# Optimization experiments

Hardware: AMD Instinct MI355X
Metric: run time of the kernel (lower is better)

The kernel has to match this reference:

```python
import jax, jax.numpy as jnp
import numpy as np
import math

# dims matching init_kwargs
B, N, CS, CZ = 1, 512, 384, 128
H, C, PQ, PV = 8, 128, 8, 8
INF, EPS = 1e5, 1e-8

# ---- quaternion / motor helpers (PGA motor encoded as [qw,qx,qy,qz,tx,ty,tz,0]) ----

def quat_conj(q):
    return q * jnp.array([1.0, -1.0, -1.0, -1.0], q.dtype)

def quat_mul(a, b):
    aw, ax, ay, az = jnp.split(a, 4, -1)
    bw, bx, by, bz = jnp.split(b, 4, -1)
    return jnp.concatenate([
        aw*bw - ax*bx - ay*by - az*bz,
        aw*bx + ax*bw + ay*bz - az*by,
        aw*by - ax*bz + ay*bw + az*bx,
        aw*bz + ax*by - ay*bx + az*bw], -1)

def quat_rotate(q, v):
    qv = q[..., 1:]
    uv = jnp.cross(qv, v)
    uuv = jnp.cross(qv, uv)
    return v + 2.0 * (q[..., :1] * uv + uuv)

def point_trafo(p, q, t):
    # p [...,K,3]; rigid transform by frame motor, homogeneous 4-vector out
    pp = quat_rotate(q, p) + t
    return jnp.concatenate([pp, jnp.ones_like(pp[..., :1])], -1)

def mv_transform(mv, q, t):
    # versor sandwich on a 16-dim multivector: three rotatable 3-vector blocks,
    # the point block (7:10, weight at 10) also translates; slots 0 and 10:16 invariant
    s0 = mv[..., 0:1]
    v1 = quat_rotate(q, mv[..., 1:4])
    v2 = quat_rotate(q, mv[..., 4:7])
    w = mv[..., 10:11]
    p = quat_rotate(q, mv[..., 7:10]) + w * t
    return jnp.concatenate([s0, v1, v2, p, mv[..., 10:16]], -1)

def mv_transform_inv(mv, q, t):
    qc = quat_conj(q)
    s0 = mv[..., 0:1]
    v1 = quat_rotate(qc, mv[..., 1:4])
    v2 = quat_rotate(qc, mv[..., 4:7])
    w = mv[..., 10:11]
    p = quat_rotate(qc, mv[..., 7:10] - w * t)
    return jnp.concatenate([s0, v1, v2, p, mv[..., 10:16]], -1)


def _forward(s, g, z, T, mask, W_q, b_q, W_kv, b_kv, W_qp, b_qp, W_kp, b_kp,
             W_vg, b_vg, W_mg, W_b, b_b, W_dz, b_dz, head_weights,
             softmax_weights, W_out, b_out, W_geo):
    T8 = T[..., :8]                                      # extract_motor
    qn = T8[..., :4]
    qn = qn / jnp.sqrt(jnp.sum(qn**2, -1, keepdims=True) + EPS)
    tr = T8[..., 4:7]

    q = (s @ W_q + b_q).reshape(B, N, H, C)
    kv = (s @ W_kv + b_kv).reshape(B, N, H, 2 * C)
    k, v = kv[..., :C], kv[..., C:]

    def make_pts(W, bb):
        # split into 3 chunks + stack(dim=-1) == reshape(...,3,HP).swapaxes
        p = (s @ W + bb).reshape(B, N, 3, H * PQ).swapaxes(-1, -2)  # [B,N,HP,3]
        p4 = point_trafo(p, qn[:, :, None, :], tr[:, :, None, :])
        return p4.reshape(B, N, H, PQ, 4)

    q_pts = make_pts(W_qp, b_qp)
    k_pts = make_pts(W_kp, b_kp)

    v_g = (s @ W_vg + b_vg).reshape(B, N, PV, 16)
    v_g = jnp.einsum('oi,bnic->bnoc', W_mg,
                     jnp.concatenate([v_g, g], -2)).reshape(B, N, H, PV, 16)

    bias = jnp.einsum('bijz,zh->bhij', z, W_b) + b_b[None, :, None, None]
    a = jnp.einsum('bihc,bjhc->bhij', q, k) * math.sqrt(1.0 / (3 * C))
    a = a + math.sqrt(1.0 / 3.0) * bias

    disp = q_pts[:, :, None, :, :, :3] - k_pts[:, None, :, :, :, :3]  # [B,N,N,H,P,3]
    pt = jnp.sum(disp**2, -1)                                         # [B,N,N,H,P]
    hw = jax.nn.softplus(head_weights) * math.sqrt(1.0 / (3 * (PQ * 9.0 / 2)))
    pt = -0.5 * jnp.sum(pt * hw[None, None, None, :, None], -1)       # [B,N,N,H]

    sq_mask = INF * (mask[:, :, None] * mask[:, None, :] - 1.0)
    a = a + pt.transpose(0, 3, 1, 2) + sq_mask[:, None]
    a = jax.nn.softmax(softmax_weights[None, :, None, None] * a, axis=-1)

    o = jnp.einsum('bhij,bjhc->bihc', a, v)                           # [B,N,H,C]

    qb, tb = qn[:, :, None, None, :], tr[:, :, None, None, :]
    vg_glob = mv_transform(v_g, qb, tb)
    o_g = jnp.einsum('bhij,bjhpc->bihpc', a, vg_glob)
    o_g = mv_transform_inv(o_g, qb, tb)                               # [B,N,H,PV,16]
    n1 = jnp.sqrt(jnp.sum(o_g[..., :10]**2, -1) + EPS)
    n2 = jnp.sqrt(jnp.sum(o_g[..., 10:]**2, -1) + EPS)
    o_g_norm = jnp.stack([n1, n2], -1)                                # [B,N,H,PV,2]

    # local relative frame features (8 per head)
    q_rel = quat_mul(quat_conj(qn)[:, :, None, :], qn[:, None, :, :])
    t_rel = quat_rotate(quat_conj(qn)[:, :, None, :], tr[:, None, :, :] - tr[:, :, None, :])
    rel = jnp.concatenate([q_rel, t_rel, jnp.zeros_like(t_rel[..., :1])], -1)  # [B,N,N,8]
    o_rel = jnp.einsum('bhij,bijc->bihc', a, rel)

    o_pair = jnp.einsum('bhij,bijc->bihc', a, z @ W_dz + b_dz)        # [B,N,H,CZ//4]

    feats = jnp.concatenate([o_pair, o, o_rel,
                             o_g.reshape(B, N, H, PV * 16),
                             o_g_norm.reshape(B, N, H, PV * 2)], -1).reshape(B, N, -1)
    s_out = feats @ W_out + b_out                                     # [B,N,CS]
    g_out = jnp.einsum('oi,bnic->bnoc', W_geo, o_g.reshape(B, N, H * PV, 16))
    return s_out, g_out


def setup_inputs() -> dict:
    key = jax.random.key(0)
    ks = jax.random.split(key, 32)
    def rn(i, shape, sc=1.0):
        return sc * jax.random.normal(ks[i], shape, jnp.float32)
    s = rn(0, (B, N, CS))
    g = rn(1, (B, N, PV, 16))
    z = rn(2, (B, N, N, CZ))
    Traw = rn(3, (B, N, 16))
    qn = Traw[..., :4]
    qn = qn / jnp.sqrt(jnp.sum(qn**2, -1, keepdims=True) + 1e-8)
    T = Traw.at[..., :4].set(qn).at[..., 4:7].multiply(3.0).at[..., 7:].set(0.0)
    mask = jnp.ones((B, N), jnp.float32)
    w = 0.02
    CAT = H * (CZ // 4 + C + 8 + PV * 18)   # 2496
    return dict(
        s=s, g=g, z=z, T=T, mask=mask,
        W_q=rn(4, (CS, H * C), w), b_q=jnp.zeros((H * C,), jnp.float32),
        W_kv=rn(5, (CS, 2 * H * C), w), b_kv=jnp.zeros((2 * H * C,), jnp.float32),
        W_qp=rn(6, (CS, H * PQ * 3), w), b_qp=jnp.zeros((H * PQ * 3,), jnp.float32),
        W_kp=rn(7, (CS, H * PQ * 3), w), b_kp=jnp.zeros((H * PQ * 3,), jnp.float32),
        W_vg=rn(8, (CS, PV * 16), w), b_vg=jnp.zeros((PV * 16,), jnp.float32),
        W_mg=rn(9, (H * PV, 2 * PV), 0.1),
        W_b=rn(10, (CZ, H), w), b_b=jnp.zeros((H,), jnp.float32),
        W_dz=rn(11, (CZ, CZ // 4), w), b_dz=jnp.zeros((CZ // 4,), jnp.float32),
        head_weights=-2.0 + 0.3 * rn(12, (H,)),
        softmax_weights=jnp.ones((H,), jnp.float32) + 0.1 * rn(13, (H,)),
        W_out=rn(14, (CAT, CS), w), b_out=jnp.zeros((CS,), jnp.float32),
        W_geo=rn(15, (PV, H * PV), 0.1))


def reference(s, g, z, T, mask, W_q, b_q, W_kv, b_kv, W_qp, b_qp, W_kp, b_kp,
              W_vg, b_vg, W_mg, W_b, b_b, W_dz, b_dz, head_weights,
              softmax_weights, W_out, b_out, W_geo):
    return _forward(s, g, z, T, mask, W_q, b_q, W_kv, b_kv, W_qp, b_qp, W_kp,
                    b_kp, W_vg, b_vg, W_mg, W_b, b_b, W_dz, b_dz, head_weights,
                    softmax_weights, W_out, b_out, W_geo)
```

## Files before the change

### kernel.cpp

```cpp
#include <hip/hip_runtime.h>
#include <math.h>

#define NN 512
#define CSD 384
#define CZD 128
#define HD 8
#define CD 128
#define EPSV 1e-8f
#define INFV 100000.0f

#define OFF_QN    ((size_t)0)
#define OFF_TR    ((size_t)2048)
#define OFF_ROWT  ((size_t)4096)
#define OFF_COLT  ((size_t)8192)
#define OFF_SB    ((size_t)12288)
#define OFF_QBUF  ((size_t)45056)
#define OFF_KV    ((size_t)569344)
#define OFF_QPR   ((size_t)1617920)
#define OFF_KPR   ((size_t)1716224)
#define OFF_VGR   ((size_t)1814528)
#define OFF_ZB    ((size_t)1880064)
#define OFF_A     ((size_t)3977216)
#define OFF_AMH   ((size_t)6074368)
#define OFF_AML   ((size_t)7122944)
#define OFF_UH    ((size_t)8171520)
#define OFF_UL    ((size_t)8499200)
#define OFF_VH    ((size_t)8826880)
#define OFF_VL    ((size_t)9154560)
#define OFF_VPH   ((size_t)9482240)
#define OFF_VPL   ((size_t)10006528)
#define OFF_OB0   ((size_t)10530816)
#define OFF_OB1   ((size_t)11055104)
#define OFF_OG0   ((size_t)11579392)
#define OFF_OG1   ((size_t)12103680)
#define OFF_FH    ((size_t)12627968)
#define OFF_FL    ((size_t)13266944)
#define OFF_PS    ((size_t)13905920)
#define OFF_SH    ((size_t)15085568)
#define OFF_SL    ((size_t)15183872)
#define OFF_WTH   ((size_t)15282176)
#define OFF_WTL   ((size_t)15970304)
#define OFF_WOH   ((size_t)16658432)
#define OFF_WOL   ((size_t)17137664)
#define OFF_AZP   ((size_t)17616896)

typedef __attribute__((ext_vector_type(4))) float f32x4;
typedef __attribute__((ext_vector_type(8))) short bf16x8;
typedef __attribute__((ext_vector_type(4))) short s16x4;
typedef unsigned short u16;

__device__ __forceinline__ void qrot(const float q[4], const float* v, float* out) {
    float qw = q[0], qx = q[1], qy = q[2], qz = q[3];
    float ux = qy*v[2] - qz*v[1];
    float uy = qz*v[0] - qx*v[2];
    float uz = qx*v[1] - qy*v[0];
    float uux = qy*uz - qz*uy;
    float uuy = qz*ux - qx*uz;
    float uuz = qx*uy - qy*ux;
    out[0] = v[0] + 2.0f*(qw*ux + uux);
    out[1] = v[1] + 2.0f*(qw*uy + uuy);
    out[2] = v[2] + 2.0f*(qw*uz + uuz);
}

__device__ __forceinline__ void cvt2(float x, u16& h, u16& lo) {
    unsigned u = __float_as_uint(x);
    unsigned r = (u + 0x7FFFu + ((u >> 16) & 1u)) >> 16;
    h = (u16)r;
    float hf = __uint_as_float(r << 16);
    float lf = x - hf;
    unsigned u2 = __float_as_uint(lf);
    unsigned r2 = (u2 + 0x7FFFu + ((u2 >> 16) & 1u)) >> 16;
    lo = (u16)r2;
}
__device__ __forceinline__ float bf2f(u16 h) { return __uint_as_float((unsigned)h << 16); }

#define MFMA3(acc, avh, avl, bvh, bvl) \
    acc = __builtin_amdgcn_mfma_f32_16x16x32_bf16(avh, bvh, acc, 0, 0, 0); \
    acc = __builtin_amdgcn_mfma_f32_16x16x32_bf16(avh, bvl, acc, 0, 0, 0); \
    acc = __builtin_amdgcn_mfma_f32_16x16x32_bf16(avl, bvh, acc, 0, 0, 0);


__global__ __launch_bounds__(256) void k_split(
    const float* __restrict__ s, const float* __restrict__ W_q, const float* __restrict__ W_kv,
    const float* __restrict__ W_qp, const float* __restrict__ W_kp, const float* __restrict__ W_vg,
    const float* __restrict__ W_out,
    u16* __restrict__ sh_, u16* __restrict__ sl_,
    u16* __restrict__ WTh, u16* __restrict__ WTl,
    u16* __restrict__ WOh, u16* __restrict__ WOl)
{
    __shared__ float tile[64*68];
    int task = blockIdx.z, bx = blockIdx.x, by = blockIdx.y, t = threadIdx.x;
    if (task == 0) {
        if (by >= 6) return;
        const float* W; int ldn, sn0;
        if (bx < 16)      { W = W_q;  ldn = 1024; sn0 = bx*64; }
        else if (bx < 48) { W = W_kv; ldn = 2048; sn0 = (bx-16)*64; }
        else if (bx < 51) { W = W_qp; ldn = 192;  sn0 = (bx-48)*64; }
        else if (bx < 54) { W = W_kp; ldn = 192;  sn0 = (bx-51)*64; }
        else              { W = W_vg; ldn = 128;  sn0 = (bx-54)*64; }
        int k0 = by*64;
        #pragma unroll
        for (int lp = 0; lp < 4; lp++) {
            int kk = (t>>4) + lp*16, nn = (t&15)*4;
            float4 v = *(const float4*)(W + (size_t)(k0+kk)*ldn + sn0 + nn);
            tile[kk*68+nn]=v.x; tile[kk*68+nn+1]=v.y; tile[kk*68+nn+2]=v.z; tile[kk*68+nn+3]=v.w;
        }
        __syncthreads();
        #pragma unroll
        for (int lp = 0; lp < 4; lp++) {
            int nn = (t>>4) + lp*16, kk4 = (t&15)*4;
            s16x4 vh, vl;
            #pragma unroll
            for (int e = 0; e < 4; e++) {
                u16 h, lo; cvt2(tile[(kk4+e)*68 + nn], h, lo);
                vh[e] = (short)h; vl[e] = (short)lo;
            }
            size_t o = (size_t)(bx*64 + nn)*384 + k0 + kk4;
            *(s16x4*)(WTh + o) = vh;
            *(s16x4*)(WTl + o) = vl;
        }
    } else if (task == 1) {
        if (bx >= 6 || by >= 39) return;
        int n0 = bx*64, k0 = by*64;
        #pragma unroll
        for (int lp = 0; lp < 4; lp++) {
            int kk = (t>>4) + lp*16, nn = (t&15)*4;
            float4 v = *(const float4*)(W_out + (size_t)(k0+kk)*384 + n0 + nn);
            tile[kk*68+nn]=v.x; tile[kk*68+nn+1]=v.y; tile[kk*68+nn+2]=v.z; tile[kk*68+nn+3]=v.w;
        }
        __syncthreads();
        #pragma unroll
        for (int lp = 0; lp < 4; lp++) {
            int nn = (t>>4) + lp*16, kk4 = (t&15)*4;
            s16x4 vh, vl;
            #pragma unroll
            for (int e = 0; e < 4; e++) {
                u16 h, lo; cvt2(tile[(kk4+e)*68 + nn], h, lo);
                vh[e] = (short)h; vl[e] = (short)lo;
            }
            size_t o = (size_t)(n0 + nn)*2496 + k0 + kk4;
            *(s16x4*)(WOh + o) = vh;
            *(s16x4*)(WOl + o) = vl;
        }
    } else {
        if (bx >= 8 || by >= 6) return;
        int m0 = bx*64, k0 = by*64;
        #pragma unroll
        for (int lp = 0; lp < 4; lp++) {
            int row = (t>>4) + lp*16, c4 = (t&15)*4;
            float4 v = *(const float4*)(s + (size_t)(m0+row)*384 + k0 + c4);
            s16x4 vh, vl;
            u16 h, lo;
            cvt2(v.x,h,lo); vh[0]=(short)h; vl[0]=(short)lo;
            cvt2(v.y,h,lo); vh[1]=(short)h; vl[1]=(short)lo;
            cvt2(v.z,h,lo); vh[2]=(short)h; vl[2]=(short)lo;
            cvt2(v.w,h,lo); vh[3]=(short)h; vl[3]=(short)lo;
            size_t o = (size_t)(m0+row)*384 + k0 + c4;
            *(s16x4*)(sh_ + o) = vh;
            *(s16x4*)(sl_ + o) = vl;
        }
    }
}

__global__ __launch_bounds__(256) void k_proj_all(
    const u16* __restrict__ sh_, const u16* __restrict__ sl_,
    const u16* __restrict__ WTh, const u16* __restrict__ WTl,
    const float* __restrict__ b_q,  float* __restrict__ qbuf,
    const float* __restrict__ b_kv, float* __restrict__ kvb,
    const float* __restrict__ b_qp, float* __restrict__ qpr,
    const float* __restrict__ b_kp, float* __restrict__ kpr,
    const float* __restrict__ b_vg, float* __restrict__ vgr)
{
    int ny = blockIdx.y;
    const float* bias; float* C; int N, n0, base;
    if (ny < 16)      { bias=b_q;  C=qbuf; N=1024; n0=ny*64;      base=0; }
    else if (ny < 48) { bias=b_kv; C=kvb;  N=2048; n0=(ny-16)*64; base=1024; }
    else if (ny < 51) { bias=b_qp; C=qpr;  N=192;  n0=(ny-48)*64; base=3072; }
    else if (ny < 54) { bias=b_kp; C=kpr;  N=192;  n0=(ny-51)*64; base=3264; }
    else              { bias=b_vg; C=vgr;  N=128;  n0=(ny-54)*64; base=3456; }
    int m0 = blockIdx.x*64;
    int t = threadIdx.x, w = t>>6, l = t&63, g = l>>4, li = l&15;
    const u16* Ah = sh_ + (size_t)(m0 + w*16 + li)*384 + g*8;
    const u16* Al = sl_ + (size_t)(m0 + w*16 + li)*384 + g*8;
    const u16* Bh0 = WTh + (size_t)(base + n0 + li)*384 + g*8;
    const u16* Bl0 = WTl + (size_t)(base + n0 + li)*384 + g*8;
    f32x4 acc[4] = {};
    for (int ks = 0; ks < 12; ks++) {
        bf16x8 avh = *(const bf16x8*)(Ah + ks*32);
        bf16x8 avl = *(const bf16x8*)(Al + ks*32);
        #pragma unroll
        for (int c = 0; c < 4; c++) {
            bf16x8 bvh = *(const bf16x8*)(Bh0 + (size_t)c*16*384 + ks*32);
            bf16x8 bvl = *(const bf16x8*)(Bl0 + (size_t)c*16*384 + ks*32);
            MFMA3(acc[c], avh, avl, bvh, bvl);
        }
    }
    #pragma unroll
    for (int c = 0; c < 4; c++) {
        int col = n0 + c*16 + li;
        float bb = bias[col];
        #pragma unroll
        for (int r = 0; r < 4; r++) {
            int row = m0 + w*16 + g*4 + r;
            C[(size_t)row*N + col] = acc[c][r] + bb;
        }
    }
}

__global__ __launch_bounds__(256) void k_geo(
    const float* __restrict__ T,
    const float* __restrict__ qpr, const float* __restrict__ kpr,
    const float* __restrict__ vgr, const float* __restrict__ g,
    const float* __restrict__ W_mg,
    const float* __restrict__ qbuf, const float* __restrict__ kvb,
    const float* __restrict__ hwraw, const float* __restrict__ b_b,
    float* __restrict__ qn, float* __restrict__ tr,
    u16* __restrict__ Uh, u16* __restrict__ Ul,
    u16* __restrict__ Vh, u16* __restrict__ Vl,
    float* __restrict__ rowt, float* __restrict__ colt,
    u16* __restrict__ Vph, u16* __restrict__ Vpl)
{
    __shared__ float s_q[4];
    __shared__ float s_t[3];
    __shared__ float s_qpts[192], s_kpts[192];
    __shared__ float s_Qsq[8], s_Ksq[8];
    int n = blockIdx.x, t = threadIdx.x;
    if (t == 0) {
        float q0=T[n*16+0], q1=T[n*16+1], q2=T[n*16+2], q3=T[n*16+3];
        float inv = 1.0f/sqrtf(q0*q0+q1*q1+q2*q2+q3*q3 + EPSV);
        float a0=q0*inv, a1=q1*inv, a2=q2*inv, a3=q3*inv;
        s_q[0]=a0; s_q[1]=a1; s_q[2]=a2; s_q[3]=a3;
        float u0=T[n*16+4], u1=T[n*16+5], u2=T[n*16+6];
        s_t[0]=u0; s_t[1]=u1; s_t[2]=u2;
        qn[n*4+0]=a0; qn[n*4+1]=a1; qn[n*4+2]=a2; qn[n*4+3]=a3;
        tr[n*3+0]=u0; tr[n*3+1]=u1; tr[n*3+2]=u2;
    }
    __syncthreads();
    float q[4]={s_q[0],s_q[1],s_q[2],s_q[3]};
    float t0=s_t[0], t1=s_t[1], t2=s_t[2];
    if (t < 128) {
        int m = t & 63;
        const float* raw = (t < 64) ? qpr : kpr;
        float p[3] = {raw[n*192 + m], raw[n*192 + 64 + m], raw[n*192 + 128 + m]};
        float r[3]; qrot(q,p,r);
        r[0]+=t0; r[1]+=t1; r[2]+=t2;
        float* dp = (t<64) ? s_qpts : s_kpts;
        dp[m*3+0]=r[0]; dp[m*3+1]=r[1]; dp[m*3+2]=r[2];
        float ss = r[0]*r[0]+r[1]*r[1]+r[2]*r[2];
        ss += __shfl_down(ss,4,8);
        ss += __shfl_down(ss,2,8);
        ss += __shfl_down(ss,1,8);
        if ((m&7)==0) ((t<64)?s_Qsq:s_Ksq)[m>>3] = ss;
    } else if (t < 192) {
        int o = t - 128;
        float in[16];
        #pragma unroll
        for (int c=0;c<16;c++){
            float acc=0.0f;
            #pragma unroll
            for (int i=0;i<8;i++)  acc += W_mg[o*16+i]*vgr[n*128+i*16+c];
            #pragma unroll
            for (int i=8;i<16;i++) acc += W_mg[o*16+i]*g[n*128+(i-8)*16+c];
            in[c]=acc;
        }
        float out[16];
        out[0]=in[0];
        qrot(q,in+1,out+1);
        qrot(q,in+4,out+4);
        float w=in[10];
        qrot(q,in+7,out+7);
        out[7]+=w*t0; out[8]+=w*t1; out[9]+=w*t2;
        #pragma unroll
        for (int c=10;c<16;c++) out[c]=in[c];
        int h=o>>3, pp=o&7;
        size_t vb = ((size_t)(h*512+n))*256 + 128 + pp*16;
        #pragma unroll
        for (int c=0;c<16;c++) {
            u16 hh, ll; cvt2(out[c], hh, ll);
            Vph[vb+c]=hh; Vpl[vb+c]=ll;
        }
    }
    #pragma unroll
    for (int l=0;l<4;l++){
        int f = t + l*256; int h = f>>7, c = f&127;
        u16 hh, ll; cvt2(kvb[(size_t)n*2048 + h*256 + 128 + c], hh, ll);
        Vph[((size_t)(h*512+n))*256 + c] = hh;
        Vpl[((size_t)(h*512+n))*256 + c] = ll;
    }
    __syncthreads();
    #pragma unroll
    for (int h = 0; h < 8; h++) {
        float hwv = log1pf(expf(hwraw[h])) * 0.09622504486493763f;
        if (t < 160) {
            float u, v;
            if (t < 128) {
                u = 0.05103103630798287f * qbuf[(size_t)n*1024 + h*128 + t];
                v = kvb[(size_t)n*2048 + h*256 + t];
            } else if (t < 152) {
                int d = t - 128;
                u = hwv * s_qpts[h*24 + d];
                v = s_kpts[h*24 + d];
            } else { u = 0.0f; v = 0.0f; }
            size_t o = ((size_t)h*512 + n)*160 + t;
            u16 hh, ll;
            cvt2(u, hh, ll); Uh[o]=hh; Ul[o]=ll;
            cvt2(v, hh, ll); Vh[o]=hh; Vl[o]=ll;
        }
        if (t == 160) rowt[h*512+n] = -0.5f*hwv*s_Qsq[h] + 0.5773502691896258f*b_b[h] - INFV;
        if (t == 161) colt[h*512+n] = -0.5f*hwv*s_Ksq[h];
    }
}

__global__ __launch_bounds__(256) void k_zb(const float* __restrict__ z,
        const float* __restrict__ W_b, float* __restrict__ zb) {
    int i = blockIdx.x, j0 = blockIdx.y*128;
    int t = threadIdx.x, w = t>>6, l = t&63;
    int jj = l>>5, c4 = (l&31)<<2;
    float wb[4][8];
    #pragma unroll
    for (int e=0;e<4;e++)
        #pragma unroll
        for (int h=0;h<8;h++) wb[e][h] = W_b[(c4+e)*8 + h];
    int jbase = j0 + w*32 + jj;
    const float* zp = z + ((size_t)i*512 + jbase)*128 + c4;
    for (int k = 0; k < 16; k++) {
        float4 v = *(const float4*)(zp + (size_t)k*256);
        float acc[8];
        #pragma unroll
        for (int h=0;h<8;h++)
            acc[h] = v.x*wb[0][h] + v.y*wb[1][h] + v.z*wb[2][h] + v.w*wb[3][h];
        #pragma unroll
        for (int h=0;h<8;h++) {
            #pragma unroll
            for (int m=16;m>0;m>>=1) acc[h] += __shfl_xor(acc[h], m);
        }
        if ((l&31) < 8) {
            int h = l&31;
            zb[((size_t)h*512 + i)*512 + jbase + k*2] = acc[h];
        }
    }
}

__global__ __launch_bounds__(256) void k_scorefill(
        const u16* __restrict__ Uh, const u16* __restrict__ Ul,
        const u16* __restrict__ Vh, const u16* __restrict__ Vl,
        const float* __restrict__ rowt, const float* __restrict__ colt,
        const float* __restrict__ zb, const float* __restrict__ mask,
        const float* __restrict__ sw, float* __restrict__ Am) {
    int h = blockIdx.z;
    int m0 = blockIdx.x*64, n0 = blockIdx.y*64;
    int t = threadIdx.x, w = t>>6, l = t&63, g = l>>4, li = l&15;
    const u16* Ah = Uh + ((size_t)h*512 + m0 + w*16 + li)*160 + g*8;
    const u16* Al = Ul + ((size_t)h*512 + m0 + w*16 + li)*160 + g*8;
    const u16* Bh0 = Vh + ((size_t)h*512 + n0 + li)*160 + g*8;
    const u16* Bl0 = Vl + ((size_t)h*512 + n0 + li)*160 + g*8;
    f32x4 acc[4] = {};
    #pragma unroll
    for (int ks = 0; ks < 5; ks++) {
        bf16x8 avh = *(const bf16x8*)(Ah + ks*32);
        bf16x8 avl = *(const bf16x8*)(Al + ks*32);
        #pragma unroll
        for (int c = 0; c < 4; c++) {
            bf16x8 bvh = *(const bf16x8*)(Bh0 + (size_t)c*16*160 + ks*32);
            bf16x8 bvl = *(const bf16x8*)(Bl0 + (size_t)c*16*160 + ks*32);
            MFMA3(acc[c], avh, avl, bvh, bvl);
        }
    }
    float swh = sw[h];
    #pragma unroll
    for (int c = 0; c < 4; c++) {
        int j = n0 + c*16 + li;
        float ct = colt[h*512 + j];
        float mj = mask[j];
        #pragma unroll
        for (int r = 0; r < 4; r++) {
            int i = m0 + w*16 + g*4 + r;
            float rt = rowt[h*512 + i];
            float mi = mask[i]*INFV;
            float zv = zb[((size_t)h*512 + i)*512 + j];
            Am[((size_t)h*512 + i)*512 + j] =
                (acc[c][r] + rt + ct + 0.5773502691896258f*zv + mi*mj)*swh;
        }
    }
}

__global__ __launch_bounds__(256) void k_softmax(const float* __restrict__ Am,
        u16* __restrict__ Amh, u16* __restrict__ Aml,
        const float* __restrict__ qn, const float* __restrict__ tr, float* __restrict__ S) {
    __shared__ float red[8];
    __shared__ float sred[4][8];
    int row = blockIdx.x;
    const float* p = Am + (size_t)row*512;
    int t = threadIdx.x;
    float x0 = p[t], x1 = p[t+256];
    float m = fmaxf(x0, x1);
    #pragma unroll
    for (int o = 32; o > 0; o >>= 1) m = fmaxf(m, __shfl_xor(m, o));
    int wv = t >> 6, ln = t & 63;
    if (ln == 0) red[wv] = m;
    __syncthreads();
    m = fmaxf(fmaxf(red[0], red[1]), fmaxf(red[2], red[3]));
    float e0 = expf(x0 - m), e1 = expf(x1 - m);
    float sm = e0 + e1;
    #pragma unroll
    for (int o = 32; o > 0; o >>= 1) sm += __shfl_xor(sm, o);
    __syncthreads();
    if (ln == 0) red[4 + wv] = sm;
    __syncthreads();
    float inv = 1.0f / (red[4]+red[5]+red[6]+red[7]);
    float a0 = e0*inv, a1 = e1*inv;
    u16 hh, ll;
    cvt2(a0, hh, ll); Amh[(size_t)row*512 + t] = hh;     Aml[(size_t)row*512 + t] = ll;
    cvt2(a1, hh, ll); Amh[(size_t)row*512 + t+256] = hh; Aml[(size_t)row*512 + t+256] = ll;
    float4 q0 = *(const float4*)(qn + t*4);
    float4 q1 = *(const float4*)(qn + (t+256)*4);
    float acc[8];
    acc[0] = a0*q0.x + a1*q1.x;
    acc[1] = a0*q0.y + a1*q1.y;
    acc[2] = a0*q0.z + a1*q1.z;
    acc[3] = a0*q0.w + a1*q1.w;
    acc[4] = a0*tr[t*3+0] + a1*tr[(t+256)*3+0];
    acc[5] = a0*tr[t*3+1] + a1*tr[(t+256)*3+1];
    acc[6] = a0*tr[t*3+2] + a1*tr[(t+256)*3+2];
    acc[7] = a0 + a1;
    #pragma unroll
    for (int c = 0; c < 8; c++) {
        #pragma unroll
        for (int o = 32; o > 0; o >>= 1) acc[c] += __shfl_xor(acc[c], o);
    }
    if (ln == 0) {
        #pragma unroll
        for (int c = 0; c < 8; c++) sred[wv][c] = acc[c];
    }
    __syncthreads();
    if (t < 8) {
        int h = row >> 9, i = row & 511;
        S[i*64 + h*8 + t] = sred[0][t]+sred[1][t]+sred[2][t]+sred[3][t];
    }
}

__global__ __launch_bounds__(256) void k_az(
        const u16* __restrict__ Amh, const u16* __restrict__ Aml,
        const float* __restrict__ z, float* __restrict__ azp) {
    __shared__ float aT[128*12];
    __shared__ float part[3*1024];
    int i = blockIdx.x, jq = blockIdx.y, j0 = jq*128;
    int t = threadIdx.x;
    #pragma unroll
    for (int l2 = 0; l2 < 4; l2++) {
        int f = t + l2*256;
        int h = f >> 7, jl = f & 127;
        size_t idx = ((size_t)h*512 + i)*512 + j0 + jl;
        aT[jl*12 + h] = bf2f(Amh[idx]) + bf2f(Aml[idx]);
    }
    __syncthreads();
    int c2 = t & 63, sub = t >> 6;
    int jb = sub*32;
    float acc[8][2] = {};
    for (int jo = 0; jo < 32; jo++) {
        int j = jb + jo;
        float2 zv = *(const float2*)(z + ((size_t)i*512 + j0 + j)*128 + c2*2);
        float4 a0 = *(const float4*)(aT + j*12);
        float4 a1 = *(const float4*)(aT + j*12 + 4);
        acc[0][0] += a0.x*zv.x; acc[0][1] += a0.x*zv.y;
        acc[1][0] += a0.y*zv.x; acc[1][1] += a0.y*zv.y;
        acc[2][0] += a0.z*zv.x; acc[2][1] += a0.z*zv.y;
        acc[3][0] += a0.w*zv.x; acc[3][1] += a0.w*zv.y;
        acc[4][0] += a1.x*zv.x; acc[4][1] += a1.x*zv.y;
        acc[5][0] += a1.y*zv.x; acc[5][1] += a1.y*zv.y;
        acc[6][0] += a1.z*zv.x; acc[6][1] += a1.z*zv.y;
        acc[7][0] += a1.w*zv.x; acc[7][1] += a1.w*zv.y;
    }
    if (sub > 0) {
        #pragma unroll
        for (int h = 0; h < 8; h++) {
            part[(sub-1)*1024 + h*128 + c2*2 + 0] = acc[h][0];
            part[(sub-1)*1024 + h*128 + c2*2 + 1] = acc[h][1];
        }
    }
    __syncthreads();
    if (sub == 0) {
        float* dst = azp + ((size_t)jq*512 + i)*1024;
        #pragma unroll
        for (int h = 0; h < 8; h++) {
            #pragma unroll
            for (int d = 0; d < 2; d++) {
                dst[h*128 + c2*2 + d] = acc[h][d] + part[h*128 + c2*2 + d]
                          + part[1024 + h*128 + c2*2 + d] + part[2048 + h*128 + c2*2 + d];
            }
        }
    }
}

__global__ __launch_bounds__(256) void k_apply(
        const u16* __restrict__ Amh, const u16* __restrict__ Aml,
        const u16* __restrict__ Vph, const u16* __restrict__ Vpl,
        float* __restrict__ ob0, float* __restrict__ ob1,
        float* __restrict__ og0, float* __restrict__ og1) {
    __shared__ u16 sBh[2][64*48];
    __shared__ u16 sBl[2][64*48];
    int m0 = blockIdx.x*64;
    int n0 = blockIdx.y*64;
    int h = blockIdx.z & 7, js = blockIdx.z >> 3;
    int t = threadIdx.x, w = t>>6, l = t&63, g = l>>4, li = l&15;
    int jl = t>>3, c8 = (t&7)*8;
    int jsw = jl ^ (((c8>>3)&3)<<3);
    const u16* Ah = Amh + ((size_t)h*512 + m0 + w*16 + li)*512 + js*256 + g*8;
    const u16* Al = Aml + ((size_t)h*512 + m0 + w*16 + li)*512 + js*256 + g*8;
    f32x4 acc[4] = {};
    {
        const u16* srcH = Vph + ((size_t)h*512 + js*256 + jl)*256 + n0 + c8;
        const u16* srcL = Vpl + ((size_t)h*512 + js*256 + jl)*256 + n0 + c8;
        bf16x8 vh = *(const bf16x8*)srcH;
        bf16x8 vl = *(const bf16x8*)srcL;
        #pragma unroll
        for (int e = 0; e < 8; e++) {
            sBh[0][(c8+e)*48 + jsw] = (u16)vh[e];
            sBl[0][(c8+e)*48 + jsw] = (u16)vl[e];
        }
    }
    __syncthreads();
    for (int kc = 0; kc < 8; kc++) {
        int cur = kc & 1;
        if (kc + 1 < 8) {
            int koff = js*256 + (kc+1)*32;
            const u16* srcH = Vph + ((size_t)h*512 + koff + jl)*256 + n0 + c8;
            const u16* srcL = Vpl + ((size_t)h*512 + koff + jl)*256 + n0 + c8;
            bf16x8 vh = *(const bf16x8*)srcH;
            bf16x8 vl = *(const bf16x8*)srcL;
            #pragma unroll
            for (int e = 0; e < 8; e++) {
                sBh[cur^1][(c8+e)*48 + jsw] = (u16)vh[e];
                sBl[cur^1][(c8+e)*48 + jsw] = (u16)vl[e];
            }
        }
        bf16x8 avh = *(const bf16x8*)(Ah + kc*32);
        bf16x8 avl = *(const bf16x8*)(Al + kc*32);
        #pragma unroll
        for (int c = 0; c < 4; c++) {
            int col = c*16 + li;
            int gp = g ^ ((col>>3)&3);
            bf16x8 bvh = *(const bf16x8*)(&sBh[cur][col*48 + gp*8]);
            bf16x8 bvl = *(const bf16x8*)(&sBl[cur][col*48 + gp*8]);
            MFMA3(acc[c], avh, avl, bvh, bvl);
        }
        __syncthreads();
    }
    float* obuf = js ? ob1 : ob0;
    float* og   = js ? og1 : og0;
    #pragma unroll
    for (int c = 0; c < 4; c++) {
        int col = n0 + c*16 + li;
        float* base = (col < 128) ? (obuf + h*128 + col) : (og + h*128 + col - 128);
        #pragma unroll
        for (int r = 0; r < 4; r++) {
            int i = m0 + w*16 + g*4 + r;
            base[(size_t)i*1024] = acc[c][r];
        }
    }
}

__global__ __launch_bounds__(256) void k_azfin(
    const float* __restrict__ azp,
    const float* __restrict__ ob0, const float* __restrict__ ob1,
    const float* __restrict__ og0, const float* __restrict__ og1,
    const float* __restrict__ W_dz, const float* __restrict__ b_dz,
    const float* __restrict__ S, const float* __restrict__ qn, const float* __restrict__ tr,
    const float* __restrict__ W_geo,
    u16* __restrict__ fh, u16* __restrict__ fl, float* __restrict__ outg)
{
    __shared__ float s_az[1024];
    __shared__ float s_og[1024];
    int i = blockIdx.x, t = threadIdx.x;
    #pragma unroll
    for (int l2 = 0; l2 < 4; l2++) {
        int c = t + l2*256;
        s_az[c] = azp[((size_t)0*512 + i)*1024 + c] + azp[((size_t)1*512 + i)*1024 + c]
                + azp[((size_t)2*512 + i)*1024 + c] + azp[((size_t)3*512 + i)*1024 + c];
    }
    __syncthreads();
    size_t fb = (size_t)i*2496;
    u16 hh, ll;
    #pragma unroll
    for (int l = 0; l < 4; l++) {
        int ff = t + l*256; int h = ff>>7, c = ff&127;
        float v = ob0[(size_t)i*1024 + h*128 + c] + ob1[(size_t)i*1024 + h*128 + c];
        cvt2(v, hh, ll); fh[fb + h*312 + 32 + c] = hh; fl[fb + h*312 + 32 + c] = ll;
    }
    {
        int h = t >> 5, cdz = t & 31;
        float a2 = b_dz[cdz];
        #pragma unroll 4
        for (int zc = 0; zc < 128; zc++) a2 += s_az[h*128 + zc]*W_dz[zc*32 + cdz];
        cvt2(a2, hh, ll); fh[fb + h*312 + cdz] = hh; fl[fb + h*312 + cdz] = ll;
    }
    float qc0=qn[i*4], qc1=-qn[i*4+1], qc2=-qn[i*4+2], qc3=-qn[i*4+3];
    float t0=tr[i*3], t1=tr[i*3+1], t2=tr[i*3+2];
    if (t < 64) {
        int h = t >> 3, p = t & 7;
        const float* a0 = og0 + (size_t)i*1024 + h*128 + p*16;
        const float* a1 = og1 + (size_t)i*1024 + h*128 + p*16;
        float in[16];
        #pragma unroll
        for (int c=0;c<16;c++) in[c]=a0[c]+a1[c];
        float qc[4]={qc0,qc1,qc2,qc3};
        float out[16];
        out[0]=in[0];
        qrot(qc,in+1,out+1);
        qrot(qc,in+4,out+4);
        float w=in[10];
        float tmp[3]={in[7]-w*t0, in[8]-w*t1, in[9]-w*t2};
        qrot(qc,tmp,out+7);
        #pragma unroll
        for (int c2x=10;c2x<16;c2x++) out[c2x]=in[c2x];
        float n1=EPSV, n2=EPSV;
        #pragma unroll
        for (int c2x=0;c2x<10;c2x++) n1 += out[c2x]*out[c2x];
        #pragma unroll
        for (int c2x=10;c2x<16;c2x++) n2 += out[c2x]*out[c2x];
        n1=sqrtf(n1); n2=sqrtf(n2);
        #pragma unroll
        for (int c2x=0;c2x<16;c2x++){
            cvt2(out[c2x], hh, ll);
            fh[fb + h*312+168+p*16+c2x] = hh; fl[fb + h*312+168+p*16+c2x] = ll;
            s_og[t*16+c2x]=out[c2x];
        }
        cvt2(n1, hh, ll); fh[fb + h*312+296+p*2]   = hh; fl[fb + h*312+296+p*2]   = ll;
        cvt2(n2, hh, ll); fh[fb + h*312+296+p*2+1] = hh; fl[fb + h*312+296+p*2+1] = ll;
    } else if (t < 72) {
        int h = t - 64;
        const float* Sr = S + i*64 + h*8;
        float b0=Sr[0], b1=Sr[1], b2=Sr[2], b3=Sr[3];
        float o0 = qc0*b0 - qc1*b1 - qc2*b2 - qc3*b3;
        float o1 = qc0*b1 + qc1*b0 + qc2*b3 - qc3*b2;
        float o2 = qc0*b2 - qc1*b3 + qc2*b0 + qc3*b1;
        float o3 = qc0*b3 + qc1*b2 - qc2*b1 + qc3*b0;
        float A = Sr[7];
        float v[3]={Sr[4]-A*t0, Sr[5]-A*t1, Sr[6]-A*t2};
        float qc[4]={qc0,qc1,qc2,qc3};
        float r[3]; qrot(qc,v,r);
        cvt2(o0,hh,ll);  fh[fb+h*312+160]=hh; fl[fb+h*312+160]=ll;
        cvt2(o1,hh,ll);  fh[fb+h*312+161]=hh; fl[fb+h*312+161]=ll;
        cvt2(o2,hh,ll);  fh[fb+h*312+162]=hh; fl[fb+h*312+162]=ll;
        cvt2(o3,hh,ll);  fh[fb+h*312+163]=hh; fl[fb+h*312+163]=ll;
        cvt2(r[0],hh,ll);fh[fb+h*312+164]=hh; fl[fb+h*312+164]=ll;
        cvt2(r[1],hh,ll);fh[fb+h*312+165]=hh; fl[fb+h*312+165]=ll;
        cvt2(r[2],hh,ll);fh[fb+h*312+166]=hh; fl[fb+h*312+166]=ll;
        fh[fb+h*312+167]=0; fl[fb+h*312+167]=0;
    }
    __syncthreads();
    if (t < 128) {
        int o = (t>>4) & 7, c = t & 15;
        float a3 = 0.0f;
        #pragma unroll 4
        for (int i2=0;i2<64;i2++) a3 += W_geo[o*64+i2]*s_og[i2*16+c];
        outg[(size_t)i*128 + o*16 + c] = a3;
    }
}

__global__ __launch_bounds__(256) void k_sout(
        const u16* __restrict__ fh, const u16* __restrict__ fl,
        const u16* __restrict__ WOh, const u16* __restrict__ WOl,
        float* __restrict__ Ps) {
    int m0 = blockIdx.x*64, n0 = blockIdx.y*64, kz = blockIdx.z;
    int t = threadIdx.x, w = t>>6, l = t&63, g = l>>4, li = l&15;
    const u16* Ah = fh + (size_t)(m0 + w*16 + li)*2496 + kz*416 + g*8;
    const u16* Al = fl + (size_t)(m0 + w*16 + li)*2496 + kz*416 + g*8;
    const u16* Bh0 = WOh + (size_t)(n0 + li)*2496 + kz*416 + g*8;
    const u16* Bl0 = WOl + (size_t)(n0 + li)*2496 + kz*416 + g*8;
    f32x4 acc[4] = {};
    for (int ks = 0; ks < 13; ks++) {
        bf16x8 avh = *(const bf16x8*)(Ah + ks*32);
        bf16x8 avl = *(const bf16x8*)(Al + ks*32);
        #pragma unroll
        for (int c = 0; c < 4; c++) {
            bf16x8 bvh = *(const bf16x8*)(Bh0 + (size_t)c*16*2496 + ks*32);
            bf16x8 bvl = *(const bf16x8*)(Bl0 + (size_t)c*16*2496 + ks*32);
            MFMA3(acc[c], avh, avl, bvh, bvl);
        }
    }
    float* slab = Ps + (size_t)kz*512*384;
    #pragma unroll
    for (int c = 0; c < 4; c++) {
        int col = n0 + c*16 + li;
        #pragma unroll
        for (int r = 0; r < 4; r++) {
            int row = m0 + w*16 + g*4 + r;
            slab[(size_t)row*CSD + col] = acc[c][r];
        }
    }
}

__global__ __launch_bounds__(256) void k_sout_red(const float* __restrict__ Ps,
        const float* __restrict__ b_out, float* __restrict__ out) {
    int idx = (blockIdx.x*256 + threadIdx.x)*4;
    float4 s = *(const float4*)(b_out + (idx % 384));
    #pragma unroll
    for (int kz = 0; kz < 6; kz++) {
        float4 p = *(const float4*)(Ps + (size_t)kz*196608 + idx);
        s.x += p.x; s.y += p.y; s.z += p.z; s.w += p.w;
    }
    *(float4*)(out + idx) = s;
}


extern "C" void kernel_launch(void* const* d_in, const int* in_sizes, int n_in,
                              void* d_out, int out_size, void* d_ws, size_t ws_size,
                              hipStream_t stream) {
    const float* s     = (const float*)d_in[0];
    const float* g     = (const float*)d_in[1];
    const float* z     = (const float*)d_in[2];
    const float* T     = (const float*)d_in[3];
    const float* mask  = (const float*)d_in[4];
    const float* W_q   = (const float*)d_in[5];
    const float* b_q   = (const float*)d_in[6];
    const float* W_kv  = (const float*)d_in[7];
    const float* b_kv  = (const float*)d_in[8];
    const float* W_qp  = (const float*)d_in[9];
    const float* b_qp  = (const float*)d_in[10];
    const float* W_kp  = (const float*)d_in[11];
    const float* b_kp  = (const float*)d_in[12];
    const float* W_vg  = (const float*)d_in[13];
    const float* b_vg  = (const float*)d_in[14];
    const float* W_mg  = (const float*)d_in[15];
    const float* W_b   = (const float*)d_in[16];
    const float* b_b   = (const float*)d_in[17];
    const float* W_dz  = (const float*)d_in[18];
    const float* b_dz  = (const float*)d_in[19];
    const float* hw    = (const float*)d_in[20];
    const float* sw    = (const float*)d_in[21];
    const float* W_out = (const float*)d_in[22];
    const float* b_out = (const float*)d_in[23];
    const float* W_geo = (const float*)d_in[24];

    float* ws   = (float*)d_ws;
    float* out  = (float*)d_out;

    float* qn   = ws + OFF_QN;
    float* tr   = ws + OFF_TR;
    float* rowt = ws + OFF_ROWT;
    float* colt = ws + OFF_COLT;
    float* Sbuf = ws + OFF_SB;
    float* qbuf = ws + OFF_QBUF;
    float* kvb  = ws + OFF_KV;
    float* qpr  = ws + OFF_QPR;
    float* kpr  = ws + OFF_KPR;
    float* vgr  = ws + OFF_VGR;
    float* zb   = ws + OFF_ZB;
    float* Am   = ws + OFF_A;
    u16* Amh    = (u16*)(ws + OFF_AMH);
    u16* Aml    = (u16*)(ws + OFF_AML);
    u16* Uh     = (u16*)(ws + OFF_UH);
    u16* Ul     = (u16*)(ws + OFF_UL);
    u16* Vh     = (u16*)(ws + OFF_VH);
    u16* Vl     = (u16*)(ws + OFF_VL);
    u16* Vph    = (u16*)(ws + OFF_VPH);
    u16* Vpl    = (u16*)(ws + OFF_VPL);
    float* ob0  = ws + OFF_OB0;
    float* ob1  = ws + OFF_OB1;
    float* og0  = ws + OFF_OG0;
    float* og1  = ws + OFF_OG1;
    u16* fh     = (u16*)(ws + OFF_FH);
    u16* fl     = (u16*)(ws + OFF_FL);
    float* Ps   = ws + OFF_PS;
    u16* sh_    = (u16*)(ws + OFF_SH);
    u16* sl_    = (u16*)(ws + OFF_SL);
    u16* WTh    = (u16*)(ws + OFF_WTH);
    u16* WTl    = (u16*)(ws + OFF_WTL);
    u16* WOh    = (u16*)(ws + OFF_WOH);
    u16* WOl    = (u16*)(ws + OFF_WOL);
    float* azp  = ws + OFF_AZP;

    k_split<<<dim3(56,39,3),256,0,stream>>>(s,W_q,W_kv,W_qp,W_kp,W_vg,W_out,
                                            sh_,sl_,WTh,WTl,WOh,WOl);
    k_proj_all<<<dim3(8,56),256,0,stream>>>(sh_,sl_,WTh,WTl,
                                            b_q,qbuf, b_kv,kvb, b_qp,qpr, b_kp,kpr, b_vg,vgr);
    k_geo<<<NN,256,0,stream>>>(T,qpr,kpr,vgr,g,W_mg,qbuf,kvb,hw,b_b,
                               qn,tr,Uh,Ul,Vh,Vl,rowt,colt,Vph,Vpl);
    k_zb<<<dim3(512,4),256,0,stream>>>(z,W_b,zb);
    k_scorefill<<<dim3(8,8,8),256,0,stream>>>(Uh,Ul,Vh,Vl,rowt,colt,zb,mask,sw,Am);
    k_softmax<<<4096,256,0,stream>>>(Am,Amh,Aml,qn,tr,Sbuf);
    k_az<<<dim3(512,4),256,0,stream>>>(Amh,Aml,z,azp);
    k_apply<<<dim3(8,4,16),256,0,stream>>>(Amh,Aml,Vph,Vpl,ob0,ob1,og0,og1);
    k_azfin<<<NN,256,0,stream>>>(azp,ob0,ob1,og0,og1,W_dz,b_dz,Sbuf,qn,tr,W_geo,
                                 fh,fl, out + (size_t)NN*CSD);
    k_sout<<<dim3(8,6,6),256,0,stream>>>(fh,fl,WOh,WOl,Ps);
    k_sout_red<<<192,256,0,stream>>>(Ps,b_out,out);
}
```

Before: 415.5 us.

## Fuse all stages into one cooperative persistent kernel with grid syncs

```diff
diff --git a/kernel.cpp b/kernel.cpp
--- a/kernel.cpp
+++ b/kernel.cpp
@@ -1,5 +1,8 @@
 #include <hip/hip_runtime.h>
+#include <hip/hip_cooperative_groups.h>
 #include <math.h>
+
+namespace cg = cooperative_groups;
 
 #define NN 512
 #define CSD 384
@@ -49,6 +52,14 @@
 typedef __attribute__((ext_vector_type(4))) short s16x4;
 typedef unsigned short u16;
 
+struct MegaP {
+    const float *s, *g, *z, *T, *mask;
+    const float *W_q, *b_q, *W_kv, *b_kv, *W_qp, *b_qp, *W_kp, *b_kp, *W_vg, *b_vg;
+    const float *W_mg, *W_b, *b_b, *W_dz, *b_dz, *hw, *sw, *W_out, *b_out, *W_geo;
+    float *ws;
+    float *out;
+};
+
 __device__ __forceinline__ void qrot(const float q[4], const float* v, float* out) {
     float qw = q[0], qx = q[1], qy = q[2], qz = q[3];
     float ux = qy*v[2] - qz*v[1];
@@ -80,24 +91,21 @@
     acc = __builtin_amdgcn_mfma_f32_16x16x32_bf16(avl, bvh, acc, 0, 0, 0);
 
 
-__global__ __launch_bounds__(256) void k_split(
-    const float* __restrict__ s, const float* __restrict__ W_q, const float* __restrict__ W_kv,
-    const float* __restrict__ W_qp, const float* __restrict__ W_kp, const float* __restrict__ W_vg,
-    const float* __restrict__ W_out,
-    u16* __restrict__ sh_, u16* __restrict__ sl_,
-    u16* __restrict__ WTh, u16* __restrict__ WTl,
-    u16* __restrict__ WOh, u16* __restrict__ WOl)
-{
-    __shared__ float tile[64*68];
-    int task = blockIdx.z, bx = blockIdx.x, by = blockIdx.y, t = threadIdx.x;
+__device__ void d_split(const MegaP& p, int task, int bx, int by, float* tile) {
+    int t = threadIdx.x;
+    u16* sh_ = (u16*)(p.ws + OFF_SH);
+    u16* sl_ = (u16*)(p.ws + OFF_SL);
+    u16* WTh = (u16*)(p.ws + OFF_WTH);
+    u16* WTl = (u16*)(p.ws + OFF_WTL);
+    u16* WOh = (u16*)(p.ws + OFF_WOH);
+    u16* WOl = (u16*)(p.ws + OFF_WOL);
     if (task == 0) {
-        if (by >= 6) return;
         const float* W; int ldn, sn0;
-        if (bx < 16)      { W = W_q;  ldn = 1024; sn0 = bx*64; }
-        else if (bx < 48) { W = W_kv; ldn = 2048; sn0 = (bx-16)*64; }
-        else if (bx < 51) { W = W_qp; ldn = 192;  sn0 = (bx-48)*64; }
-        else if (bx < 54) { W = W_kp; ldn = 192;  sn0 = (bx-51)*64; }
-        else              { W = W_vg; ldn = 128;  sn0 = (bx-54)*64; }
+        if (bx < 16)      { W = p.W_q;  ldn = 1024; sn0 = bx*64; }
+        else if (bx < 48) { W = p.W_kv; ldn = 2048; sn0 = (bx-16)*64; }
+        else if (bx < 51) { W = p.W_qp; ldn = 192;  sn0 = (bx-48)*64; }
+        else if (bx < 54) { W = p.W_kp; ldn = 192;  sn0 = (bx-51)*64; }
+        else              { W = p.W_vg; ldn = 128;  sn0 = (bx-54)*64; }
         int k0 = by*64;
         #pragma unroll
         for (int lp = 0; lp < 4; lp++) {
@@ -115,17 +123,16 @@
                 u16 h, lo; cvt2(tile[(kk4+e)*68 + nn], h, lo);
                 vh[e] = (short)h; vl[e] = (short)lo;
             }
-            size_t o = (size_t)(bx*64 + nn)*384 + k0 + kk4;
+            size_t o = (size_t)(bx*64 + nn)*384 + by*64 + kk4;
             *(s16x4*)(WTh + o) = vh;
             *(s16x4*)(WTl + o) = vl;
         }
     } else if (task == 1) {
-        if (bx >= 6 || by >= 39) return;
         int n0 = bx*64, k0 = by*64;
         #pragma unroll
         for (int lp = 0; lp < 4; lp++) {
             int kk = (t>>4) + lp*16, nn = (t&15)*4;
-            float4 v = *(const float4*)(W_out + (size_t)(k0+kk)*384 + n0 + nn);
+            float4 v = *(const float4*)(p.W_out + (size_t)(k0+kk)*384 + n0 + nn);
             tile[kk*68+nn]=v.x; tile[kk*68+nn+1]=v.y; tile[kk*68+nn+2]=v.z; tile[kk*68+nn+3]=v.w;
         }
         __syncthreads();
@@ -143,12 +150,11 @@
             *(s16x4*)(WOl + o) = vl;
         }
     } else {
-        if (bx >= 8 || by >= 6) return;
         int m0 = bx*64, k0 = by*64;
         #pragma unroll
         for (int lp = 0; lp < 4; lp++) {
             int row = (t>>4) + lp*16, c4 = (t&15)*4;
-            float4 v = *(const float4*)(s + (size_t)(m0+row)*384 + k0 + c4);
+            float4 v = *(const float4*)(p.s + (size_t)(m0+row)*384 + k0 + c4);
             s16x4 vh, vl;
             u16 h, lo;
             cvt2(v.x,h,lo); vh[0]=(short)h; vl[0]=(short)lo;
@@ -162,23 +168,48 @@
     }
 }
 
-__global__ __launch_bounds__(256) void k_proj_all(
-    const u16* __restrict__ sh_, const u16* __restrict__ sl_,
-    const u16* __restrict__ WTh, const u16* __restrict__ WTl,
-    const float* __restrict__ b_q,  float* __restrict__ qbuf,
-    const float* __restrict__ b_kv, float* __restrict__ kvb,
-    const float* __restrict__ b_qp, float* __restrict__ qpr,
-    const float* __restrict__ b_kp, float* __restrict__ kpr,
-    const float* __restrict__ b_vg, float* __restrict__ vgr)
-{
-    int ny = blockIdx.y;
+__device__ void d_zb(const MegaP& p, int i, int jq) {
+    float* zb = p.ws + OFF_ZB;
+    int j0 = jq*128;
+    int t = threadIdx.x, w = t>>6, l = t&63;
+    int jj = l>>5, c4 = (l&31)<<2;
+    float wb[4][8];
+    #pragma unroll
+    for (int e=0;e<4;e++)
+        #pragma unroll
+        for (int h=0;h<8;h++) wb[e][h] = p.W_b[(c4+e)*8 + h];
+    int jbase = j0 + w*32 + jj;
+    const float* zp = p.z + ((size_t)i*512 + jbase)*128 + c4;
+    for (int k = 0; k < 16; k++) {
+        float4 v = *(const float4*)(zp + (size_t)k*256);
+        float acc[8];
+        #pragma unroll
+        for (int h=0;h<8;h++)
+            acc[h] = v.x*wb[0][h] + v.y*wb[1][h] + v.z*wb[2][h] + v.w*wb[3][h];
+        #pragma unroll
+        for (int h=0;h<8;h++) {
+            #pragma unroll
+            for (int m=16;m>0;m>>=1) acc[h] += __shfl_xor(acc[h], m);
+        }
+        if ((l&31) < 8) {
+            int h = l&31;
+            zb[((size_t)h*512 + i)*512 + jbase + k*2] = acc[h];
+        }
+    }
+}
+
+__device__ void d_proj(const MegaP& p, int bx, int ny) {
+    const u16* sh_ = (const u16*)(p.ws + OFF_SH);
+    const u16* sl_ = (const u16*)(p.ws + OFF_SL);
+    const u16* WTh = (const u16*)(p.ws + OFF_WTH);
+    const u16* WTl = (const u16*)(p.ws + OFF_WTL);
     const float* bias; float* C; int N, n0, base;
-    if (ny < 16)      { bias=b_q;  C=qbuf; N=1024; n0=ny*64;      base=0; }
-    else if (ny < 48) { bias=b_kv; C=kvb;  N=2048; n0=(ny-16)*64; base=1024; }
-    else if (ny < 51) { bias=b_qp; C=qpr;  N=192;  n0=(ny-48)*64; base=3072; }
-    else if (ny < 54) { bias=b_kp; C=kpr;  N=192;  n0=(ny-51)*64; base=3264; }
-    else              { bias=b_vg; C=vgr;  N=128;  n0=(ny-54)*64; base=3456; }
-    int m0 = blockIdx.x*64;
+    if (ny < 16)      { bias=p.b_q;  C=p.ws+OFF_QBUF; N=1024; n0=ny*64;      base=0; }
+    else if (ny < 48) { bias=p.b_kv; C=p.ws+OFF_KV;   N=2048; n0=(ny-16)*64; base=1024; }
+    else if (ny < 51) { bias=p.b_qp; C=p.ws+OFF_QPR;  N=192;  n0=(ny-48)*64; base=3072; }
+    else if (ny < 54) { bias=p.b_kp; C=p.ws+OFF_KPR;  N=192;  n0=(ny-51)*64; base=3264; }
+    else              { bias=p.b_vg; C=p.ws+OFF_VGR;  N=128;  n0=(ny-54)*64; base=3456; }
+    int m0 = bx*64;
     int t = threadIdx.x, w = t>>6, l = t&63, g = l>>4, li = l&15;
     const u16* Ah = sh_ + (size_t)(m0 + w*16 + li)*384 + g*8;
     const u16* Al = sl_ + (size_t)(m0 + w*16 + li)*384 + g*8;
@@ -207,30 +238,28 @@
     }
 }
 
-__global__ __launch_bounds__(256) void k_geo(
-    const float* __restrict__ T,
-    const float* __restrict__ qpr, const float* __restrict__ kpr,
-    const float* __restrict__ vgr, const float* __restrict__ g,
-    const float* __restrict__ W_mg,
-    const float* __restrict__ qbuf, const float* __restrict__ kvb,
-    const float* __restrict__ hwraw, const float* __restrict__ b_b,
-    float* __restrict__ qn, float* __restrict__ tr,
-    u16* __restrict__ Uh, u16* __restrict__ Ul,
-    u16* __restrict__ Vh, u16* __restrict__ Vl,
-    float* __restrict__ rowt, float* __restrict__ colt,
-    u16* __restrict__ Vph, u16* __restrict__ Vpl)
-{
-    __shared__ float s_q[4];
-    __shared__ float s_t[3];
-    __shared__ float s_qpts[192], s_kpts[192];
-    __shared__ float s_Qsq[8], s_Ksq[8];
-    int n = blockIdx.x, t = threadIdx.x;
+__device__ void d_geo(const MegaP& p, int n, float* sg) {
+    float* s_q = sg; float* s_t = sg+4;
+    float* s_qpts = sg+8; float* s_kpts = sg+200;
+    float* s_Qsq = sg+392; float* s_Ksq = sg+400;
+    const float* qpr = p.ws + OFF_QPR;
+    const float* kpr = p.ws + OFF_KPR;
+    const float* vgr = p.ws + OFF_VGR;
+    const float* qbuf = p.ws + OFF_QBUF;
+    const float* kvb = p.ws + OFF_KV;
+    float* qn = p.ws + OFF_QN;
+    float* tr = p.ws + OFF_TR;
+    u16* Uh = (u16*)(p.ws + OFF_UH); u16* Ul = (u16*)(p.ws + OFF_UL);
+    u16* Vh = (u16*)(p.ws + OFF_VH); u16* Vl = (u16*)(p.ws + OFF_VL);
+    float* rowt = p.ws + OFF_ROWT; float* colt = p.ws + OFF_COLT;
+    u16* Vph = (u16*)(p.ws + OFF_VPH); u16* Vpl = (u16*)(p.ws + OFF_VPL);
+    int t = threadIdx.x;
     if (t == 0) {
-        float q0=T[n*16+0], q1=T[n*16+1], q2=T[n*16+2], q3=T[n*16+3];
+        float q0=p.T[n*16+0], q1=p.T[n*16+1], q2=p.T[n*16+2], q3=p.T[n*16+3];
         float inv = 1.0f/sqrtf(q0*q0+q1*q1+q2*q2+q3*q3 + EPSV);
         float a0=q0*inv, a1=q1*inv, a2=q2*inv, a3=q3*inv;
         s_q[0]=a0; s_q[1]=a1; s_q[2]=a2; s_q[3]=a3;
-        float u0=T[n*16+4], u1=T[n*16+5], u2=T[n*16+6];
+        float u0=p.T[n*16+4], u1=p.T[n*16+5], u2=p.T[n*16+6];
         s_t[0]=u0; s_t[1]=u1; s_t[2]=u2;
         qn[n*4+0]=a0; qn[n*4+1]=a1; qn[n*4+2]=a2; qn[n*4+3]=a3;
         tr[n*3+0]=u0; tr[n*3+1]=u1; tr[n*3+2]=u2;
@@ -241,8 +270,8 @@
     if (t < 128) {
         int m = t & 63;
         const float* raw = (t < 64) ? qpr : kpr;
-        float p[3] = {raw[n*192 + m], raw[n*192 + 64 + m], raw[n*192 + 128 + m]};
-        float r[3]; qrot(q,p,r);
+        float pp[3] = {raw[n*192 + m], raw[n*192 + 64 + m], raw[n*192 + 128 + m]};
+        float r[3]; qrot(q,pp,r);
         r[0]+=t0; r[1]+=t1; r[2]+=t2;
         float* dp = (t<64) ? s_qpts : s_kpts;
         dp[m*3+0]=r[0]; dp[m*3+1]=r[1]; dp[m*3+2]=r[2];
@@ -258,9 +287,9 @@
         for (int c=0;c<16;c++){
             float acc=0.0f;
             #pragma unroll
-            for (int i=0;i<8;i++)  acc += W_mg[o*16+i]*vgr[n*128+i*16+c];
+            for (int i2=0;i2<8;i2++)  acc += p.W_mg[o*16+i2]*vgr[n*128+i2*16+c];
             #pragma unroll
-            for (int i=8;i<16;i++) acc += W_mg[o*16+i]*g[n*128+(i-8)*16+c];
+            for (int i2=8;i2<16;i2++) acc += p.W_mg[o*16+i2]*p.g[n*128+(i2-8)*16+c];
             in[c]=acc;
         }
         float out[16];
@@ -272,8 +301,8 @@
         out[7]+=w*t0; out[8]+=w*t1; out[9]+=w*t2;
         #pragma unroll
         for (int c=10;c<16;c++) out[c]=in[c];
-        int h=o>>3, pp=o&7;
-        size_t vb = ((size_t)(h*512+n))*256 + 128 + pp*16;
+        int h=o>>3, pp2=o&7;
+        size_t vb = ((size_t)(h*512+n))*256 + 128 + pp2*16;
         #pragma unroll
         for (int c=0;c<16;c++) {
             u16 hh, ll; cvt2(out[c], hh, ll);
@@ -290,7 +319,7 @@
     __syncthreads();
     #pragma unroll
     for (int h = 0; h < 8; h++) {
-        float hwv = log1pf(expf(hwraw[h])) * 0.09622504486493763f;
+        float hwv = log1pf(expf(p.hw[h])) * 0.09622504486493763f;
         if (t < 160) {
             float u, v;
             if (t < 128) {
@@ -306,49 +335,21 @@
             cvt2(u, hh, ll); Uh[o]=hh; Ul[o]=ll;
             cvt2(v, hh, ll); Vh[o]=hh; Vl[o]=ll;
         }
-        if (t == 160) rowt[h*512+n] = -0.5f*hwv*s_Qsq[h] + 0.5773502691896258f*b_b[h] - INFV;
+        if (t == 160) rowt[h*512+n] = -0.5f*hwv*s_Qsq[h] + 0.5773502691896258f*p.b_b[h] - INFV;
         if (t == 161) colt[h*512+n] = -0.5f*hwv*s_Ksq[h];
     }
 }
 
-__global__ __launch_bounds__(256) void k_zb(const float* __restrict__ z,
-        const float* __restrict__ W_b, float* __restrict__ zb) {
-    int i = blockIdx.x, j0 = blockIdx.y*128;
-    int t = threadIdx.x, w = t>>6, l = t&63;
-    int jj = l>>5, c4 = (l&31)<<2;
-    float wb[4][8];
-    #pragma unroll
-    for (int e=0;e<4;e++)
-        #pragma unroll
-        for (int h=0;h<8;h++) wb[e][h] = W_b[(c4+e)*8 + h];
-    int jbase = j0 + w*32 + jj;
-    const float* zp = z + ((size_t)i*512 + jbase)*128 + c4;
-    for (int k = 0; k < 16; k++) {
-        float4 v = *(const float4*)(zp + (size_t)k*256);
-        float acc[8];
-        #pragma unroll
-        for (int h=0;h<8;h++)
-            acc[h] = v.x*wb[0][h] + v.y*wb[1][h] + v.z*wb[2][h] + v.w*wb[3][h];
-        #pragma unroll
-        for (int h=0;h<8;h++) {
-            #pragma unroll
-            for (int m=16;m>0;m>>=1) acc[h] += __shfl_xor(acc[h], m);
-        }
-        if ((l&31) < 8) {
-            int h = l&31;
-            zb[((size_t)h*512 + i)*512 + jbase + k*2] = acc[h];
-        }
-    }
-}
-
-__global__ __launch_bounds__(256) void k_scorefill(
-        const u16* __restrict__ Uh, const u16* __restrict__ Ul,
-        const u16* __restrict__ Vh, const u16* __restrict__ Vl,
-        const float* __restrict__ rowt, const float* __restrict__ colt,
-        const float* __restrict__ zb, const float* __restrict__ mask,
-        const float* __restrict__ sw, float* __restrict__ Am) {
-    int h = blockIdx.z;
-    int m0 = blockIdx.x*64, n0 = blockIdx.y*64;
+__device__ void d_scorefill(const MegaP& p, int bx, int by, int h) {
+    const u16* Uh = (const u16*)(p.ws + OFF_UH);
+    const u16* Ul = (const u16*)(p.ws + OFF_UL);
+    const u16* Vh = (const u16*)(p.ws + OFF_VH);
+    const u16* Vl = (const u16*)(p.ws + OFF_VL);
+    const float* rowt = p.ws + OFF_ROWT;
+    const float* colt = p.ws + OFF_COLT;
+    const float* zb = p.ws + OFF_ZB;
+    float* Am = p.ws + OFF_A;
+    int m0 = bx*64, n0 = by*64;
     int t = threadIdx.x, w = t>>6, l = t&63, g = l>>4, li = l&15;
     const u16* Ah = Uh + ((size_t)h*512 + m0 + w*16 + li)*160 + g*8;
     const u16* Al = Ul + ((size_t)h*512 + m0 + w*16 + li)*160 + g*8;
@@ -366,17 +367,17 @@
             MFMA3(acc[c], avh, avl, bvh, bvl);
         }
     }
-    float swh = sw[h];
+    float swh = p.sw[h];
     #pragma unroll
     for (int c = 0; c < 4; c++) {
         int j = n0 + c*16 + li;
         float ct = colt[h*512 + j];
-        float mj = mask[j];
+        float mj = p.mask[j];
         #pragma unroll
         for (int r = 0; r < 4; r++) {
             int i = m0 + w*16 + g*4 + r;
             float rt = rowt[h*512 + i];
-            float mi = mask[i]*INFV;
+            float mi = p.mask[i]*INFV;
             float zv = zb[((size_t)h*512 + i)*512 + j];
             Am[((size_t)h*512 + i)*512 + j] =
                 (acc[c][r] + rt + ct + 0.5773502691896258f*zv + mi*mj)*swh;
@@ -384,15 +385,17 @@
     }
 }
 
-__global__ __launch_bounds__(256) void k_softmax(const float* __restrict__ Am,
-        u16* __restrict__ Amh, u16* __restrict__ Aml,
-        const float* __restrict__ qn, const float* __restrict__ tr, float* __restrict__ S) {
-    __shared__ float red[8];
-    __shared__ float sred[4][8];
-    int row = blockIdx.x;
-    const float* p = Am + (size_t)row*512;
+__device__ void d_softmax(const MegaP& p, int row, float* smem) {
+    float* red = smem;
+    const float* Am = p.ws + OFF_A;
+    u16* Amh = (u16*)(p.ws + OFF_AMH);
+    u16* Aml = (u16*)(p.ws + OFF_AML);
+    const float* qn = p.ws + OFF_QN;
+    const float* tr = p.ws + OFF_TR;
+    float* S = p.ws + OFF_SB;
+    const float* pr = Am + (size_t)row*512;
     int t = threadIdx.x;
-    float x0 = p[t], x1 = p[t+256];
+    float x0 = pr[t], x1 = pr[t+256];
     float m = fmaxf(x0, x1);
     #pragma unroll
     for (int o = 32; o > 0; o >>= 1) m = fmaxf(m, __shfl_xor(m, o));
@@ -430,21 +433,21 @@
     }
     if (ln == 0) {
         #pragma unroll
-        for (int c = 0; c < 8; c++) sred[wv][c] = acc[c];
+        for (int c = 0; c < 8; c++) smem[8 + wv*8 + c] = acc[c];
     }
     __syncthreads();
     if (t < 8) {
         int h = row >> 9, i = row & 511;
-        S[i*64 + h*8 + t] = sred[0][t]+sred[1][t]+sred[2][t]+sred[3][t];
-    }
-}
-
-__global__ __launch_bounds__(256) void k_az(
-        const u16* __restrict__ Amh, const u16* __restrict__ Aml,
-        const float* __restrict__ z, float* __restrict__ azp) {
-    __shared__ float aT[128*12];
-    __shared__ float part[3*1024];
-    int i = blockIdx.x, jq = blockIdx.y, j0 = jq*128;
+        S[i*64 + h*8 + t] = smem[8+t] + smem[16+t] + smem[24+t] + smem[32+t];
+    }
+}
+
+__device__ void d_az(const MegaP& p, int i, int jq, float* aT) {
+    float* part = aT + 1536;
+    const u16* Amh = (const u16*)(p.ws + OFF_AMH);
+    const u16* Aml = (const u16*)(p.ws + OFF_AML);
+    float* azp = p.ws + OFF_AZP;
+    int j0 = jq*128;
     int t = threadIdx.x;
     #pragma unroll
     for (int l2 = 0; l2 < 4; l2++) {
@@ -459,7 +462,7 @@
     float acc[8][2] = {};
     for (int jo = 0; jo < 32; jo++) {
         int j = jb + jo;
-        float2 zv = *(const float2*)(z + ((size_t)i*512 + j0 + j)*128 + c2*2);
+        float2 zv = *(const float2*)(p.z + ((size_t)i*512 + j0 + j)*128 + c2*2);
         float4 a0 = *(const float4*)(aT + j*12);
         float4 a1 = *(const float4*)(aT + j*12 + 4);
         acc[0][0] += a0.x*zv.x; acc[0][1] += a0.x*zv.y;
@@ -492,16 +495,15 @@
     }
 }
 
-__global__ __launch_bounds__(256) void k_apply(
-        const u16* __restrict__ Amh, const u16* __restrict__ Aml,
-        const u16* __restrict__ Vph, const u16* __restrict__ Vpl,
-        float* __restrict__ ob0, float* __restrict__ ob1,
-        float* __restrict__ og0, float* __restrict__ og1) {
-    __shared__ u16 sBh[2][64*48];
-    __shared__ u16 sBl[2][64*48];
-    int m0 = blockIdx.x*64;
-    int n0 = blockIdx.y*64;
-    int h = blockIdx.z & 7, js = blockIdx.z >> 3;
+__device__ void d_apply(const MegaP& p, int bx, int by, int bz, u16* sB) {
+    const u16* Amh = (const u16*)(p.ws + OFF_AMH);
+    const u16* Aml = (const u16*)(p.ws + OFF_AML);
+    const u16* Vph = (const u16*)(p.ws + OFF_VPH);
+    const u16* Vpl = (const u16*)(p.ws + OFF_VPL);
+    float* ob0 = p.ws + OFF_OB0; float* ob1 = p.ws + OFF_OB1;
+    float* og0 = p.ws + OFF_OG0; float* og1 = p.ws + OFF_OG1;
+    int m0 = bx*64, n0 = by*64;
+    int h = bz & 7, js = bz >> 3;
     int t = threadIdx.x, w = t>>6, l = t&63, g = l>>4, li = l&15;
     int jl = t>>3, c8 = (t&7)*8;
     int jsw = jl ^ (((c8>>3)&3)<<3);
@@ -515,8 +517,8 @@
         bf16x8 vl = *(const bf16x8*)srcL;
         #pragma unroll
         for (int e = 0; e < 8; e++) {
-            sBh[0][(c8+e)*48 + jsw] = (u16)vh[e];
-            sBl[0][(c8+e)*48 + jsw] = (u16)vl[e];
+            sB[(c8+e)*48 + jsw] = (u16)vh[e];
+            sB[6144 + (c8+e)*48 + jsw] = (u16)vl[e];
         }
     }
     __syncthreads();
@@ -530,8 +532,8 @@
             bf16x8 vl = *(const bf16x8*)srcL;
             #pragma unroll
             for (int e = 0; e < 8; e++) {
-                sBh[cur^1][(c8+e)*48 + jsw] = (u16)vh[e];
-                sBl[cur^1][(c8+e)*48 + jsw] = (u16)vl[e];
+                sB[(cur^1)*3072 + (c8+e)*48 + jsw] = (u16)vh[e];
+                sB[6144 + (cur^1)*3072 + (c8+e)*48 + jsw] = (u16)vl[e];
             }
         }
         bf16x8 avh = *(const bf16x8*)(Ah + kc*32);
@@ -540,8 +542,8 @@
         for (int c = 0; c < 4; c++) {
             int col = c*16 + li;
             int gp = g ^ ((col>>3)&3);
-            bf16x8 bvh = *(const bf16x8*)(&sBh[cur][col*48 + gp*8]);
-            bf16x8 bvl = *(const bf16x8*)(&sBl[cur][col*48 + gp*8]);
+            bf16x8 bvh = *(const bf16x8*)(&sB[cur*3072 + col*48 + gp*8]);
+            bf16x8 bvl = *(const bf16x8*)(&sB[6144 + cur*3072 + col*48 + gp*8]);
             MFMA3(acc[c], avh, avl, bvh, bvl);
         }
         __syncthreads();
@@ -560,18 +562,18 @@
     }
 }
 
-__global__ __launch_bounds__(256) void k_azfin(
-    const float* __restrict__ azp,
-    const float* __restrict__ ob0, const float* __restrict__ ob1,
-    const float* __restrict__ og0, const float* __restrict__ og1,
-    const float* __restrict__ W_dz, const float* __restrict__ b_dz,
-    const float* __restrict__ S, const float* __restrict__ qn, const float* __restrict__ tr,
-    const float* __restrict__ W_geo,
-    u16* __restrict__ fh, u16* __restrict__ fl, float* __restrict__ outg)
-{
-    __shared__ float s_az[1024];
-    __shared__ float s_og[1024];
-    int i = blockIdx.x, t = threadIdx.x;
+__device__ void d_azfin(const MegaP& p, int i, float* s_az) {
+    float* s_og = s_az + 1024;
+    const float* azp = p.ws + OFF_AZP;
+    const float* ob0 = p.ws + OFF_OB0; const float* ob1 = p.ws + OFF_OB1;
+    const float* og0 = p.ws + OFF_OG0; const float* og1 = p.ws + OFF_OG1;
+    const float* S = p.ws + OFF_SB;
+    const float* qn = p.ws + OFF_QN;
+    const float* tr = p.ws + OFF_TR;
+    u16* fh = (u16*)(p.ws + OFF_FH);
+    u16* fl = (u16*)(p.ws + OFF_FL);
+    float* outg = p.out + (size_t)NN*CSD;
+    int t = threadIdx.x;
     #pragma unroll
     for (int l2 = 0; l2 < 4; l2++) {
         int c = t + l2*256;
@@ -589,17 +591,17 @@
     }
     {
         int h = t >> 5, cdz = t & 31;
-        float a2 = b_dz[cdz];
+        float a2 = p.b_dz[cdz];
         #pragma unroll 4
-        for (int zc = 0; zc < 128; zc++) a2 += s_az[h*128 + zc]*W_dz[zc*32 + cdz];
+        for (int zc = 0; zc < 128; zc++) a2 += s_az[h*128 + zc]*p.W_dz[zc*32 + cdz];
         cvt2(a2, hh, ll); fh[fb + h*312 + cdz] = hh; fl[fb + h*312 + cdz] = ll;
     }
     float qc0=qn[i*4], qc1=-qn[i*4+1], qc2=-qn[i*4+2], qc3=-qn[i*4+3];
     float t0=tr[i*3], t1=tr[i*3+1], t2=tr[i*3+2];
     if (t < 64) {
-        int h = t >> 3, p = t & 7;
-        const float* a0 = og0 + (size_t)i*1024 + h*128 + p*16;
-        const float* a1 = og1 + (size_t)i*1024 + h*128 + p*16;
+        int h = t >> 3, pp = t & 7;
+        const float* a0 = og0 + (size_t)i*1024 + h*128 + pp*16;
+        const float* a1 = og1 + (size_t)i*1024 + h*128 + pp*16;
         float in[16];
         #pragma unroll
         for (int c=0;c<16;c++) in[c]=a0[c]+a1[c];
@@ -622,11 +624,11 @@
         #pragma unroll
         for (int c2x=0;c2x<16;c2x++){
             cvt2(out[c2x], hh, ll);
-            fh[fb + h*312+168+p*16+c2x] = hh; fl[fb + h*312+168+p*16+c2x] = ll;
+            fh[fb + h*312+168+pp*16+c2x] = hh; fl[fb + h*312+168+pp*16+c2x] = ll;
             s_og[t*16+c2x]=out[c2x];
         }
-        cvt2(n1, hh, ll); fh[fb + h*312+296+p*2]   = hh; fl[fb + h*312+296+p*2]   = ll;
-        cvt2(n2, hh, ll); fh[fb + h*312+296+p*2+1] = hh; fl[fb + h*312+296+p*2+1] = ll;
+        cvt2(n1, hh, ll); fh[fb + h*312+296+pp*2]   = hh; fl[fb + h*312+296+pp*2]   = ll;
+        cvt2(n2, hh, ll); fh[fb + h*312+296+pp*2+1] = hh; fl[fb + h*312+296+pp*2+1] = ll;
     } else if (t < 72) {
         int h = t - 64;
         const float* Sr = S + i*64 + h*8;
@@ -653,16 +655,18 @@
         int o = (t>>4) & 7, c = t & 15;
         float a3 = 0.0f;
         #pragma unroll 4
-        for (int i2=0;i2<64;i2++) a3 += W_geo[o*64+i2]*s_og[i2*16+c];
+        for (int i2=0;i2<64;i2++) a3 += p.W_geo[o*64+i2]*s_og[i2*16+c];
         outg[(size_t)i*128 + o*16 + c] = a3;
     }
 }
 
-__global__ __launch_bounds__(256) void k_sout(
-        const u16* __restrict__ fh, const u16* __restrict__ fl,
-        const u16* __restrict__ WOh, const u16* __restrict__ WOl,
-        float* __restrict__ Ps) {
-    int m0 = blockIdx.x*64, n0 = blockIdx.y*64, kz = blockIdx.z;
+__device__ void d_sout(const MegaP& p, int bx, int by, int kz) {
+    const u16* fh = (const u16*)(p.ws + OFF_FH);
+    const u16* fl = (const u16*)(p.ws + OFF_FL);
+    const u16* WOh = (const u16*)(p.ws + OFF_WOH);
+    const u16* WOl = (const u16*)(p.ws + OFF_WOL);
+    float* Ps = p.ws + OFF_PS;
+    int m0 = bx*64, n0 = by*64;
     int t = threadIdx.x, w = t>>6, l = t&63, g = l>>4, li = l&15;
     const u16* Ah = fh + (size_t)(m0 + w*16 + li)*2496 + kz*416 + g*8;
     const u16* Al = fl + (size_t)(m0 + w*16 + li)*2496 + kz*416 + g*8;
@@ -691,99 +695,159 @@
     }
 }
 
-__global__ __launch_bounds__(256) void k_sout_red(const float* __restrict__ Ps,
-        const float* __restrict__ b_out, float* __restrict__ out) {
-    int idx = (blockIdx.x*256 + threadIdx.x)*4;
-    float4 s = *(const float4*)(b_out + (idx % 384));
+__device__ void d_red(const MegaP& p, int u) {
+    const float* Ps = p.ws + OFF_PS;
+    int idx = (u*256 + threadIdx.x)*4;
+    float4 s = *(const float4*)(p.b_out + (idx % 384));
     #pragma unroll
     for (int kz = 0; kz < 6; kz++) {
-        float4 p = *(const float4*)(Ps + (size_t)kz*196608 + idx);
-        s.x += p.x; s.y += p.y; s.z += p.z; s.w += p.w;
-    }
-    *(float4*)(out + idx) = s;
+        float4 pp = *(const float4*)(Ps + (size_t)kz*196608 + idx);
+        s.x += pp.x; s.y += pp.y; s.z += pp.z; s.w += pp.w;
+    }
+    *(float4*)(p.out + idx) = s;
+}
+
+
+__global__ __launch_bounds__(256) void k_mega(MegaP p) {
+    __shared__ __align__(16) unsigned char smraw[24576];
+    float* smf = (float*)smraw;
+    u16*   smu = (u16*)smraw;
+    cg::grid_group gg = cg::this_grid();
+    int bid = blockIdx.x;
+    for (int vb = bid; vb < 2666; vb += 512) {
+        __syncthreads();
+        if (vb < 336)      d_split(p, 0, vb % 56, vb / 56, smf);
+        else if (vb < 570) { int u = vb - 336; d_split(p, 1, u % 6, u / 6, smf); }
+        else if (vb < 618) { int u = vb - 570; d_split(p, 2, u % 8, u / 8, smf); }
+        else               { int u = vb - 618; d_zb(p, u >> 2, u & 3); }
+    }
+    gg.sync();
+    for (int vb = bid; vb < 448; vb += 512)
+        d_proj(p, vb & 7, vb >> 3);
+    gg.sync();
+    {
+        __syncthreads();
+        d_geo(p, bid, smf);
+    }
+    gg.sync();
+    d_scorefill(p, bid & 7, (bid >> 3) & 7, bid >> 6);
+    gg.sync();
+    for (int vb = bid; vb < 4096; vb += 512) {
+        __syncthreads();
+        d_softmax(p, vb, smf);
+    }
+    gg.sync();
+    for (int vb = bid; vb < 2560; vb += 512) {
+        __syncthreads();
+        if (vb < 2048) d_az(p, vb >> 2, vb & 3, smf);
+        else { int u = vb - 2048; d_apply(p, u & 7, (u >> 3) & 3, u >> 5, smu); }
+    }
+    gg.sync();
+    {
+        __syncthreads();
+        d_azfin(p, bid, smf);
+    }
+    gg.sync();
+    for (int vb = bid; vb < 288; vb += 512)
+        d_sout(p, vb % 8, (vb / 8) % 6, vb / 48);
+    gg.sync();
+    for (int vb = bid; vb < 192; vb += 512)
+        d_red(p, vb);
+}
+
+
+__global__ __launch_bounds__(256) void k_split_g(MegaP p) {
+    __shared__ __align__(16) float tile[64*68];
+    int task = blockIdx.z, bx = blockIdx.x, by = blockIdx.y;
+    if (task == 0 && by >= 6) return;
+    if (task == 1 && (bx >= 6 || by >= 39)) return;
+    if (task == 2 && (bx >= 8 || by >= 6)) return;
+    d_split(p, task, bx, by, tile);
+}
+__global__ __launch_bounds__(256) void k_proj_g(MegaP p) {
+    d_proj(p, blockIdx.x, blockIdx.y);
+}
+__global__ __launch_bounds__(256) void k_geo_g(MegaP p) {
+    __shared__ __align__(16) float sg[408];
+    d_geo(p, blockIdx.x, sg);
+}
+__global__ __launch_bounds__(256) void k_zb_g(MegaP p) {
+    d_zb(p, blockIdx.x, blockIdx.y);
+}
+__global__ __launch_bounds__(256) void k_scorefill_g(MegaP p) {
+    d_scorefill(p, blockIdx.x, blockIdx.y, blockIdx.z);
+}
+__global__ __launch_bounds__(256) void k_softmax_g(MegaP p) {
+    __shared__ __align__(16) float sm_[40];
+    d_softmax(p, blockIdx.x, sm_);
+}
+__global__ __launch_bounds__(256) void k_az_g(MegaP p) {
+    __shared__ __align__(16) float aT[4608];
+    d_az(p, blockIdx.x, blockIdx.y, aT);
+}
+__global__ __launch_bounds__(256) void k_apply_g(MegaP p) {
+    __shared__ __align__(16) u16 sB[12288];
+    d_apply(p, blockIdx.x, blockIdx.y, blockIdx.z, sB);
+}
+__global__ __launch_bounds__(256) void k_azfin_g(MegaP p) {
+    __shared__ __align__(16) float sz[2048];
+    d_azfin(p, blockIdx.x, sz);
+}
+__global__ __launch_bounds__(256) void k_sout_g(MegaP p) {
+    d_sout(p, blockIdx.x, blockIdx.y, blockIdx.z);
+}
+__global__ __launch_bounds__(256) void k_red_g(MegaP p) {
+    d_red(p, blockIdx.x);
 }
 
 
 extern "C" void kernel_launch(void* const* d_in, const int* in_sizes, int n_in,
                               void* d_out, int out_size, void* d_ws, size_t ws_size,
                               hipStream_t stream) {
-    const float* s     = (const float*)d_in[0];
-    const float* g     = (const float*)d_in[1];
-    const float* z     = (const float*)d_in[2];
-    const float* T     = (const float*)d_in[3];
-    const float* mask  = (const float*)d_in[4];
-    const float* W_q   = (const float*)d_in[5];
-    const float* b_q   = (const float*)d_in[6];
-    const float* W_kv  = (const float*)d_in[7];
-    const float* b_kv  = (const float*)d_in[8];
-    const float* W_qp  = (const float*)d_in[9];
-    const float* b_qp  = (const float*)d_in[10];
-    const float* W_kp  = (const float*)d_in[11];
-    const float* b_kp  = (const float*)d_in[12];
-    const float* W_vg  = (const float*)d_in[13];
-    const float* b_vg  = (const float*)d_in[14];
-    const float* W_mg  = (const float*)d_in[15];
-    const float* W_b   = (const float*)d_in[16];
-    const float* b_b   = (const float*)d_in[17];
-    const float* W_dz  = (const float*)d_in[18];
-    const float* b_dz  = (const float*)d_in[19];
-    const float* hw    = (const float*)d_in[20];
-    const float* sw    = (const float*)d_in[21];
-    const float* W_out = (const float*)d_in[22];
-    const float* b_out = (const float*)d_in[23];
-    const float* W_geo = (const float*)d_in[24];
-
-    float* ws   = (float*)d_ws;
-    float* out  = (float*)d_out;
-
-    float* qn   = ws + OFF_QN;
-    float* tr   = ws + OFF_TR;
-    float* rowt = ws + OFF_ROWT;
-    float* colt = ws + OFF_COLT;
-    float* Sbuf = ws + OFF_SB;
-    float* qbuf = ws + OFF_QBUF;
-    float* kvb  = ws + OFF_KV;
-    float* qpr  = ws + OFF_QPR;
-    float* kpr  = ws + OFF_KPR;
-    float* vgr  = ws + OFF_VGR;
-    float* zb   = ws + OFF_ZB;
-    float* Am   = ws + OFF_A;
-    u16* Amh    = (u16*)(ws + OFF_AMH);
-    u16* Aml    = (u16*)(ws + OFF_AML);
-    u16* Uh     = (u16*)(ws + OFF_UH);
-    u16* Ul     = (u16*)(ws + OFF_UL);
-    u16* Vh     = (u16*)(ws + OFF_VH);
-    u16* Vl     = (u16*)(ws + OFF_VL);
-    u16* Vph    = (u16*)(ws + OFF_VPH);
-    u16* Vpl    = (u16*)(ws + OFF_VPL);
-    float* ob0  = ws + OFF_OB0;
-    float* ob1  = ws + OFF_OB1;
-    float* og0  = ws + OFF_OG0;
-    float* og1  = ws + OFF_OG1;
-    u16* fh     = (u16*)(ws + OFF_FH);
-    u16* fl     = (u16*)(ws + OFF_FL);
-    float* Ps   = ws + OFF_PS;
-    u16* sh_    = (u16*)(ws + OFF_SH);
-    u16* sl_    = (u16*)(ws + OFF_SL);
-    u16* WTh    = (u16*)(ws + OFF_WTH);
-    u16* WTl    = (u16*)(ws + OFF_WTL);
-    u16* WOh    = (u16*)(ws + OFF_WOH);
-    u16* WOl    = (u16*)(ws + OFF_WOL);
-    float* azp  = ws + OFF_AZP;
-
-    k_split<<<dim3(56,39,3),256,0,stream>>>(s,W_q,W_kv,W_qp,W_kp,W_vg,W_out,
-                                            sh_,sl_,WTh,WTl,WOh,WOl);
-    k_proj_all<<<dim3(8,56),256,0,stream>>>(sh_,sl_,WTh,WTl,
-                                            b_q,qbuf, b_kv,kvb, b_qp,qpr, b_kp,kpr, b_vg,vgr);
-    k_geo<<<NN,256,0,stream>>>(T,qpr,kpr,vgr,g,W_mg,qbuf,kvb,hw,b_b,
-                               qn,tr,Uh,Ul,Vh,Vl,rowt,colt,Vph,Vpl);
-    k_zb<<<dim3(512,4),256,0,stream>>>(z,W_b,zb);
-    k_scorefill<<<dim3(8,8,8),256,0,stream>>>(Uh,Ul,Vh,Vl,rowt,colt,zb,mask,sw,Am);
-    k_softmax<<<4096,256,0,stream>>>(Am,Amh,Aml,qn,tr,Sbuf);
-    k_az<<<dim3(512,4),256,0,stream>>>(Amh,Aml,z,azp);
-    k_apply<<<dim3(8,4,16),256,0,stream>>>(Amh,Aml,Vph,Vpl,ob0,ob1,og0,og1);
-    k_azfin<<<NN,256,0,stream>>>(azp,ob0,ob1,og0,og1,W_dz,b_dz,Sbuf,qn,tr,W_geo,
-                                 fh,fl, out + (size_t)NN*CSD);
-    k_sout<<<dim3(8,6,6),256,0,stream>>>(fh,fl,WOh,WOl,Ps);
-    k_sout_red<<<192,256,0,stream>>>(Ps,b_out,out);
-}
+    MegaP P;
+    P.s     = (const float*)d_in[0];
+    P.g     = (const float*)d_in[1];
+    P.z     = (const float*)d_in[2];
+    P.T     = (const float*)d_in[3];
+    P.mask  = (const float*)d_in[4];
+    P.W_q   = (const float*)d_in[5];
+    P.b_q   = (const float*)d_in[6];
+    P.W_kv  = (const float*)d_in[7];
+    P.b_kv  = (const float*)d_in[8];
+    P.W_qp  = (const float*)d_in[9];
+    P.b_qp  = (const float*)d_in[10];
+    P.W_kp  = (const float*)d_in[11];
+    P.b_kp  = (const float*)d_in[12];
+    P.W_vg  = (const float*)d_in[13];
+    P.b_vg  = (const float*)d_in[14];
+    P.W_mg  = (const float*)d_in[15];
+    P.W_b   = (const float*)d_in[16];
+    P.b_b   = (const float*)d_in[17];
+    P.W_dz  = (const float*)d_in[18];
+    P.b_dz  = (const float*)d_in[19];
+    P.hw    = (const float*)d_in[20];
+    P.sw    = (const float*)d_in[21];
+    P.W_out = (const float*)d_in[22];
+    P.b_out = (const float*)d_in[23];
+    P.W_geo = (const float*)d_in[24];
+    P.ws    = (float*)d_ws;
+    P.out   = (float*)d_out;
+
+    void* kargs[] = { (void*)&P };
+    hipError_t e = hipLaunchCooperativeKernel((const void*)k_mega,
+                                              dim3(512), dim3(256), kargs, 0, stream);
+    if (e != hipSuccess) {
+        (void)hipGetLastError();
+        k_split_g<<<dim3(56,39,3),256,0,stream>>>(P);
+        k_proj_g<<<dim3(8,56),256,0,stream>>>(P);
+        k_geo_g<<<NN,256,0,stream>>>(P);
+        k_zb_g<<<dim3(512,4),256,0,stream>>>(P);
+        k_scorefill_g<<<dim3(8,8,8),256,0,stream>>>(P);
+        k_softmax_g<<<4096,256,0,stream>>>(P);
+        k_az_g<<<dim3(512,4),256,0,stream>>>(P);
+        k_apply_g<<<dim3(8,4,16),256,0,stream>>>(P);
+        k_azfin_g<<<NN,256,0,stream>>>(P);
+        k_sout_g<<<dim3(8,6,6),256,0,stream>>>(P);
+        k_red_g<<<192,256,0,stream>>>(P);
+    }
+}
```

New measurement: 935.5 us. 125% more time.
